# Kernel tuning notes

Hardware: AMD Instinct MI355X
Metric: run time of the kernel (lower is better)

## Reference

```python
import jax, jax.numpy as jnp
import numpy as np

B, S, H = 16, 8192, 256

def setup_inputs() -> dict:
    key = jax.random.key(0)
    k1, k2, k3, k4, k5 = jax.random.split(key, 5)
    hidden = jax.random.normal(k1, (B, 1, H), dtype=jnp.float32)
    encoder_outputs = jax.random.normal(k2, (B, S, 2 * H), dtype=jnp.float32)
    attn_w = jax.random.normal(k3, (H, 3 * H), dtype=jnp.float32) / np.sqrt(3 * H)
    attn_b = jax.random.normal(k4, (H,), dtype=jnp.float32) * 0.01
    v = jax.random.uniform(k5, (H,), dtype=jnp.float32)
    return {"hidden": hidden, "encoder_outputs": encoder_outputs,
            "attn_w": attn_w, "attn_b": attn_b, "v": v}

def reference(hidden, encoder_outputs, attn_w, attn_b, v):
    # Vectorized form of the per-timestep loop:
    # energies[b, s] = sum_h v[h] * tanh(Linear(cat(hidden[b], enc[b, s])))
    b, s, _ = encoder_outputs.shape
    h_bcast = jnp.broadcast_to(hidden, (b, s, hidden.shape[-1]))  # [B,S,H]
    combined = jnp.concatenate([h_bcast, encoder_outputs], axis=-1)  # [B,S,3H]
    energy = jnp.tanh(jnp.einsum('bsk,hk->bsh', combined, attn_w) + attn_b)  # [B,S,H]
    attn_energies = jnp.einsum('bsh,h->bs', energy, v)  # [B,S]
    return jax.nn.softmax(attn_energies, axis=1)[:, None, :]  # [B,1,S]
```

## Files before the change

kernel.cpp:

```cpp
#include <hip/hip_runtime.h>
#include <hip/hip_bf16.h>

#define B_ 16
#define S_ 8192
#define H_ 256
#define K_ 512
#define MT_ 64
#define NBLK (S_/MT_)

typedef __attribute__((ext_vector_type(8))) short bf16x8;
typedef __attribute__((ext_vector_type(4))) float f32x4;

static __device__ __forceinline__ unsigned short f2bf(float x) {
    __hip_bfloat16 h = __float2bfloat16(x);
    unsigned short r;
    __builtin_memcpy(&r, &h, 2);
    return r;
}

__global__ __launch_bounds__(256) void wprep_kernel(const float* __restrict__ w,
                                                    bf16x8* __restrict__ wfrag) {
    int slot = blockIdx.x * 256 + threadIdx.x;
    int lane = slot & 63;
    int ks   = (slot >> 6) & 15;
    int nt   = slot >> 10;
    int n  = (nt << 4) + (lane & 15);
    int k0 = (ks << 5) + ((lane >> 4) << 3);
    const float* src = w + n * 768 + 256 + k0;
    unsigned short u[8];
#pragma unroll
    for (int j = 0; j < 8; ++j) u[j] = f2bf(src[j]);
    uint4 p;
    p.x = (unsigned)u[0] | ((unsigned)u[1] << 16);
    p.y = (unsigned)u[2] | ((unsigned)u[3] << 16);
    p.z = (unsigned)u[4] | ((unsigned)u[5] << 16);
    p.w = (unsigned)u[6] | ((unsigned)u[7] << 16);
    ((uint4*)wfrag)[slot] = p;
}

__global__ __launch_bounds__(256) void qprep_kernel(const float* __restrict__ w,
                                                    const float* __restrict__ bias,
                                                    const float* __restrict__ hid,
                                                    float* __restrict__ q) {
    int b = blockIdx.x, h = threadIdx.x;
    const float* wr = w + h * 768;
    const float* hb = hid + b * H_;
    float acc = bias[h];
    for (int k = 0; k < H_; ++k) acc += wr[k] * hb[k];
    q[b * H_ + h] = acc;
}

__global__ __launch_bounds__(256) void energy_kernel(const float* __restrict__ enc,
                                                     const bf16x8* __restrict__ wfrag,
                                                     const float* __restrict__ qv,
                                                     const float* __restrict__ vv,
                                                     float* __restrict__ ener) {
    __shared__ char  At[MT_ * K_ * 2];
    __shared__ float epart[4][MT_];

    const int bid  = blockIdx.x;
    const int b    = bid >> 7;
    const int s0   = (bid & 127) * MT_;
    const int tid  = threadIdx.x;
    const int lane = tid & 63;
    const int wv   = tid >> 6;
    const int lr   = lane & 15;
    const int lg   = lane >> 4;

    const float* gbase = enc + ((size_t)(b * S_ + s0)) * K_;
#pragma unroll
    for (int j = 0; j < 16; ++j) {
        int chunk = j * 256 + tid;
        int row = chunk >> 6;
        int k0  = (chunk & 63) << 3;
        const float4* gp = (const float4*)(gbase + row * K_ + k0);
        float4 f0 = gp[0], f1 = gp[1];
        uint4 p;
        p.x = (unsigned)f2bf(f0.x) | ((unsigned)f2bf(f0.y) << 16);
        p.y = (unsigned)f2bf(f0.z) | ((unsigned)f2bf(f0.w) << 16);
        p.z = (unsigned)f2bf(f1.x) | ((unsigned)f2bf(f1.y) << 16);
        p.w = (unsigned)f2bf(f1.z) | ((unsigned)f2bf(f1.w) << 16);
        int lin = chunk << 4;
        int sw  = lin ^ ((row & 7) << 4);
        *(uint4*)(At + sw) = p;
    }

    float qreg[4], vreg[4];
#pragma unroll
    for (int n = 0; n < 4; ++n) {
        int col = (wv * 4 + n) * 16 + lr;
        qreg[n] = qv[b * H_ + col];
        vreg[n] = vv[col];
    }

    __syncthreads();

    f32x4 acc[4][4];
#pragma unroll
    for (int mt = 0; mt < 4; ++mt)
#pragma unroll
        for (int n = 0; n < 4; ++n)
            acc[mt][n] = (f32x4){0.f, 0.f, 0.f, 0.f};

#pragma unroll 4
    for (int ks = 0; ks < 16; ++ks) {
        bf16x8 a[4];
#pragma unroll
        for (int mt = 0; mt < 4; ++mt) {
            int row = mt * 16 + lr;
            int lin = row * 1024 + ks * 64 + lg * 16;
            int sw  = lin ^ ((row & 7) << 4);
            a[mt] = *(const bf16x8*)(At + sw);
        }
#pragma unroll
        for (int n = 0; n < 4; ++n) {
            bf16x8 bfr = wfrag[(((wv * 4 + n) * 16 + ks) << 6) + lane];
#pragma unroll
            for (int mt = 0; mt < 4; ++mt)
                acc[mt][n] = __builtin_amdgcn_mfma_f32_16x16x32_bf16(a[mt], bfr, acc[mt][n], 0, 0, 0);
        }
    }

#pragma unroll
    for (int mt = 0; mt < 4; ++mt) {
#pragma unroll
        for (int j = 0; j < 4; ++j) {
            float s = 0.f;
#pragma unroll
            for (int n = 0; n < 4; ++n)
                s += vreg[n] * tanhf(qreg[n] + acc[mt][n][j]);
            s += __shfl_xor(s, 1);
            s += __shfl_xor(s, 2);
            s += __shfl_xor(s, 4);
            s += __shfl_xor(s, 8);
            if (lr == 0) epart[wv][mt * 16 + lg * 4 + j] = s;
        }
    }
    __syncthreads();
    if (tid < MT_) {
        float s = epart[0][tid] + epart[1][tid] + epart[2][tid] + epart[3][tid];
        ener[b * S_ + s0 + tid] = s;
    }
}

__global__ __launch_bounds__(1024) void softmax_kernel(const float* __restrict__ ener,
                                                       float* __restrict__ out) {
    __shared__ float redm[16], reds[16];
    int b = blockIdx.x, tid = threadIdx.x;
    int lane = tid & 63, wv = tid >> 6;
    const float* e = ener + b * S_;
    float v[8];
#pragma unroll
    for (int i = 0; i < 8; ++i) v[i] = e[i * 1024 + tid];
    float m = v[0];
#pragma unroll
    for (int i = 1; i < 8; ++i) m = fmaxf(m, v[i]);
#pragma unroll
    for (int msk = 1; msk < 64; msk <<= 1) m = fmaxf(m, __shfl_xor(m, msk));
    if (lane == 0) redm[wv] = m;
    __syncthreads();
    float M = redm[0];
#pragma unroll
    for (int i = 1; i < 16; ++i) M = fmaxf(M, redm[i]);
    float s = 0.f;
#pragma unroll
    for (int i = 0; i < 8; ++i) { v[i] = __expf(v[i] - M); s += v[i]; }
#pragma unroll
    for (int msk = 1; msk < 64; msk <<= 1) s += __shfl_xor(s, msk);
    if (lane == 0) reds[wv] = s;
    __syncthreads();
    float T = 0.f;
#pragma unroll
    for (int i = 0; i < 16; ++i) T += reds[i];
    float inv = 1.0f / T;
    float* ob = out + b * S_;
#pragma unroll
    for (int i = 0; i < 8; ++i) ob[i * 1024 + tid] = v[i] * inv;
}

extern "C" void kernel_launch(void* const* d_in, const int* in_sizes, int n_in,
                              void* d_out, int out_size, void* d_ws, size_t ws_size,
                              hipStream_t stream) {
    const float* hidden = (const float*)d_in[0];
    const float* enc    = (const float*)d_in[1];
    const float* attn_w = (const float*)d_in[2];
    const float* attn_b = (const float*)d_in[3];
    const float* v      = (const float*)d_in[4];
    float* out = (float*)d_out;

    char* ws = (char*)d_ws;
    bf16x8* wfrag = (bf16x8*)ws;
    float*  q     = (float*)(ws + 262144);
    float*  ener  = (float*)(ws + 262144 + 16384);

    wprep_kernel<<<64, 256, 0, stream>>>(attn_w, wfrag);
    qprep_kernel<<<B_, 256, 0, stream>>>(attn_w, attn_b, hidden, q);
    energy_kernel<<<B_ * NBLK, 256, 0, stream>>>(enc, wfrag, q, v, ener);
    softmax_kernel<<<B_, 1024, 0, stream>>>(ener, out);
}
```

Baseline: 437.2 us.

## Stream encoder rows directly to MFMA registers, merge prep kernels, use fast tanh

The energy kernel no longer stages a 64x512 bf16 tile in LDS. Each wave now loads its own 16 encoder rows straight from global memory, converts them to bf16 in registers, and computes all 16 output column tiles itself, which removes the LDS writes, the LDS reads and both block barriers. The weight-fragment and q precompute kernels are merged into one vectorised launch, and tanhf is replaced by an exp/rcp approximation. In exchange, each wave now reads the whole 256 KB bf16 weight fragment from cache instead of a quarter of it, raising L2 traffic, and the fast tanh is slightly less accurate.

```diff
diff --git a/kernel.cpp b/kernel.cpp
--- a/kernel.cpp
+++ b/kernel.cpp
@@ -5,8 +5,7 @@
 #define S_ 8192
 #define H_ 256
 #define K_ 512
-#define MT_ 64
-#define NBLK (S_/MT_)
+#define NT_ 16
 
 typedef __attribute__((ext_vector_type(8))) short bf16x8;
 typedef __attribute__((ext_vector_type(4))) float f32x4;
@@ -18,36 +17,55 @@
     return r;
 }
 
-__global__ __launch_bounds__(256) void wprep_kernel(const float* __restrict__ w,
-                                                    bf16x8* __restrict__ wfrag) {
-    int slot = blockIdx.x * 256 + threadIdx.x;
-    int lane = slot & 63;
-    int ks   = (slot >> 6) & 15;
-    int nt   = slot >> 10;
-    int n  = (nt << 4) + (lane & 15);
-    int k0 = (ks << 5) + ((lane >> 4) << 3);
-    const float* src = w + n * 768 + 256 + k0;
-    unsigned short u[8];
-#pragma unroll
-    for (int j = 0; j < 8; ++j) u[j] = f2bf(src[j]);
-    uint4 p;
-    p.x = (unsigned)u[0] | ((unsigned)u[1] << 16);
-    p.y = (unsigned)u[2] | ((unsigned)u[3] << 16);
-    p.z = (unsigned)u[4] | ((unsigned)u[5] << 16);
-    p.w = (unsigned)u[6] | ((unsigned)u[7] << 16);
-    ((uint4*)wfrag)[slot] = p;
+static __device__ __forceinline__ bf16x8 pack8(float4 f0, float4 f1) {
+    bf16x8 r;
+    r[0] = (short)f2bf(f0.x); r[1] = (short)f2bf(f0.y);
+    r[2] = (short)f2bf(f0.z); r[3] = (short)f2bf(f0.w);
+    r[4] = (short)f2bf(f1.x); r[5] = (short)f2bf(f1.y);
+    r[6] = (short)f2bf(f1.z); r[7] = (short)f2bf(f1.w);
+    return r;
 }
 
-__global__ __launch_bounds__(256) void qprep_kernel(const float* __restrict__ w,
+static __device__ __forceinline__ float fast_tanh(float x) {
+    x = fminf(15.f, fmaxf(-15.f, x));
+    float e = __expf(2.f * x);
+    return 1.f - 2.f * __builtin_amdgcn_rcpf(e + 1.f);
+}
+
+__global__ __launch_bounds__(1024) void prep_kernel(const float* __restrict__ w,
                                                     const float* __restrict__ bias,
                                                     const float* __restrict__ hid,
+                                                    bf16x8* __restrict__ wfrag,
                                                     float* __restrict__ q) {
-    int b = blockIdx.x, h = threadIdx.x;
-    const float* wr = w + h * 768;
-    const float* hb = hid + b * H_;
-    float acc = bias[h];
-    for (int k = 0; k < H_; ++k) acc += wr[k] * hb[k];
-    q[b * H_ + h] = acc;
+    int blk = blockIdx.x;
+    int tid = threadIdx.x;
+    if (blk < 16) {
+        int slot = blk * 1024 + tid;
+        int lane = slot & 63;
+        int nt   = (slot >> 6) & 15;
+        int ks   = slot >> 10;
+        int n  = (nt << 4) + (lane & 15);
+        int k0 = (ks << 5) + ((lane >> 4) << 3);
+        const float* src = w + n * 768 + 256 + k0;
+        float4 f0 = *(const float4*)(src);
+        float4 f1 = *(const float4*)(src + 4);
+        wfrag[slot] = pack8(f0, f1);
+    } else {
+        int b = blk - 16;
+        int h = tid >> 2, part = tid & 3;
+        const float* wr = w + h * 768 + part * 64;
+        const float* hb = hid + b * H_ + part * 64;
+        float acc = 0.f;
+#pragma unroll
+        for (int i = 0; i < 16; ++i) {
+            float4 a = *(const float4*)(wr + i * 4);
+            float4 x = *(const float4*)(hb + i * 4);
+            acc += a.x * x.x + a.y * x.y + a.z * x.z + a.w * x.w;
+        }
+        acc += __shfl_xor(acc, 1);
+        acc += __shfl_xor(acc, 2);
+        if (part == 0) q[b * H_ + h] = acc + bias[h];
+    }
 }
 
 __global__ __launch_bounds__(256) void energy_kernel(const float* __restrict__ enc,
@@ -55,91 +73,55 @@
                                                      const float* __restrict__ qv,
                                                      const float* __restrict__ vv,
                                                      float* __restrict__ ener) {
-    __shared__ char  At[MT_ * K_ * 2];
-    __shared__ float epart[4][MT_];
-
     const int bid  = blockIdx.x;
     const int b    = bid >> 7;
-    const int s0   = (bid & 127) * MT_;
+    const int s0   = (bid & 127) * 64;
     const int tid  = threadIdx.x;
     const int lane = tid & 63;
     const int wv   = tid >> 6;
     const int lr   = lane & 15;
     const int lg   = lane >> 4;
+    const int r0   = s0 + wv * 16;
 
-    const float* gbase = enc + ((size_t)(b * S_ + s0)) * K_;
+    const float* arow = enc + ((size_t)(b * S_ + r0 + lr)) * K_ + lg * 8;
+    const bf16x8* wbase = wfrag + lane;
+
+    f32x4 acc[NT_];
 #pragma unroll
-    for (int j = 0; j < 16; ++j) {
-        int chunk = j * 256 + tid;
-        int row = chunk >> 6;
-        int k0  = (chunk & 63) << 3;
-        const float4* gp = (const float4*)(gbase + row * K_ + k0);
-        float4 f0 = gp[0], f1 = gp[1];
-        uint4 p;
-        p.x = (unsigned)f2bf(f0.x) | ((unsigned)f2bf(f0.y) << 16);
-        p.y = (unsigned)f2bf(f0.z) | ((unsigned)f2bf(f0.w) << 16);
-        p.z = (unsigned)f2bf(f1.x) | ((unsigned)f2bf(f1.y) << 16);
-        p.w = (unsigned)f2bf(f1.z) | ((unsigned)f2bf(f1.w) << 16);
-        int lin = chunk << 4;
-        int sw  = lin ^ ((row & 7) << 4);
-        *(uint4*)(At + sw) = p;
-    }
+    for (int nt = 0; nt < NT_; ++nt) acc[nt] = (f32x4){0.f, 0.f, 0.f, 0.f};
 
-    float qreg[4], vreg[4];
+#pragma unroll 2
+    for (int ks = 0; ks < 16; ++ks) {
+        float4 f0 = *(const float4*)(arow + ks * 32);
+        float4 f1 = *(const float4*)(arow + ks * 32 + 4);
+        bf16x8 a = pack8(f0, f1);
 #pragma unroll
-    for (int n = 0; n < 4; ++n) {
-        int col = (wv * 4 + n) * 16 + lr;
-        qreg[n] = qv[b * H_ + col];
-        vreg[n] = vv[col];
-    }
-
-    __syncthreads();
-
-    f32x4 acc[4][4];
-#pragma unroll
-    for (int mt = 0; mt < 4; ++mt)
-#pragma unroll
-        for (int n = 0; n < 4; ++n)
-            acc[mt][n] = (f32x4){0.f, 0.f, 0.f, 0.f};
-
-#pragma unroll 4
-    for (int ks = 0; ks < 16; ++ks) {
-        bf16x8 a[4];
-#pragma unroll
-        for (int mt = 0; mt < 4; ++mt) {
-            int row = mt * 16 + lr;
-            int lin = row * 1024 + ks * 64 + lg * 16;
-            int sw  = lin ^ ((row & 7) << 4);
-            a[mt] = *(const bf16x8*)(At + sw);
-        }
-#pragma unroll
-        for (int n = 0; n < 4; ++n) {
-            bf16x8 bfr = wfrag[(((wv * 4 + n) * 16 + ks) << 6) + lane];
-#pragma unroll
-            for (int mt = 0; mt < 4; ++mt)
-                acc[mt][n] = __builtin_amdgcn_mfma_f32_16x16x32_bf16(a[mt], bfr, acc[mt][n], 0, 0, 0);
+        for (int nt = 0; nt < NT_; ++nt) {
+            bf16x8 bf = wbase[(ks * 16 + nt) * 64];
+            acc[nt] = __builtin_amdgcn_mfma_f32_16x16x32_bf16(a, bf, acc[nt], 0, 0, 0);
         }
     }
 
+    const float* qb = qv + b * H_;
+    float e[4] = {0.f, 0.f, 0.f, 0.f};
 #pragma unroll
-    for (int mt = 0; mt < 4; ++mt) {
+    for (int nt = 0; nt < NT_; ++nt) {
+        float qn = qb[nt * 16 + lr];
+        float vn = vv[nt * 16 + lr];
 #pragma unroll
-        for (int j = 0; j < 4; ++j) {
-            float s = 0.f;
+        for (int j = 0; j < 4; ++j)
+            e[j] += vn * fast_tanh(qn + acc[nt][j]);
+    }
 #pragma unroll
-            for (int n = 0; n < 4; ++n)
-                s += vreg[n] * tanhf(qreg[n] + acc[mt][n][j]);
-            s += __shfl_xor(s, 1);
-            s += __shfl_xor(s, 2);
-            s += __shfl_xor(s, 4);
-            s += __shfl_xor(s, 8);
-            if (lr == 0) epart[wv][mt * 16 + lg * 4 + j] = s;
-        }
+    for (int j = 0; j < 4; ++j) {
+        e[j] += __shfl_xor(e[j], 1);
+        e[j] += __shfl_xor(e[j], 2);
+        e[j] += __shfl_xor(e[j], 4);
+        e[j] += __shfl_xor(e[j], 8);
     }
-    __syncthreads();
-    if (tid < MT_) {
-        float s = epart[0][tid] + epart[1][tid] + epart[2][tid] + epart[3][tid];
-        ener[b * S_ + s0 + tid] = s;
+    if (lr == 0) {
+        float* op = ener + b * S_ + r0 + lg * 4;
+        op[0] = e[0]; op[1] = e[1]; op[2] = e[2]; op[3] = e[3];
     }
 }
 
@@ -193,8 +175,7 @@
     float*  q     = (float*)(ws + 262144);
     float*  ener  = (float*)(ws + 262144 + 16384);
 
-    wprep_kernel<<<64, 256, 0, stream>>>(attn_w, wfrag);
-    qprep_kernel<<<B_, 256, 0, stream>>>(attn_w, attn_b, hidden, q);
-    energy_kernel<<<B_ * NBLK, 256, 0, stream>>>(enc, wfrag, q, v, ener);
+    prep_kernel<<<32, 1024, 0, stream>>>(attn_w, attn_b, hidden, wfrag, q);
+    energy_kernel<<<B_ * (S_ / 64), 256, 0, stream>>>(enc, wfrag, q, v, ener);
     softmax_kernel<<<B_, 1024, 0, stream>>>(ener, out);
 }
```

Result: slower. 454.4 us (+3.9%).
